# Kernel tuning notes

Hardware: AMD Instinct MI355X
Metric: run time of the kernel (lower is better)

## Reference

```python
import jax, jax.numpy as jnp
import numpy as np

D = 192          # embed_dim
DI = 2 * D       # d_inner (Mamba expand=2)
R = 12           # dt_rank = ceil(D / d_state)
N = 16           # d_state
DEPTH = 24
P = 16           # patch size
B = 4
SS, TS = 256, 128
PT = (TS // P) ** 2   # 64 template patches
PS = (SS // P) ** 2   # 256 search patches
L = PT + PS + 1       # 321 tokens (middle cls)


def setup_inputs() -> dict:
    key = jax.random.key(0)
    ks = jax.random.split(key, 24)
    f = lambda k, shp, s=0.02: (jax.random.normal(k, shp) * s).astype(jnp.float32)
    Alog = jnp.log(jnp.arange(1, N + 1, dtype=jnp.float32))  # S4D-real init
    Alog = jnp.tile(Alog, (DEPTH, DI, 1))
    return {
        "x_search": f(ks[0], (B, 3, SS, SS), 1.0),
        "x_template": f(ks[1], (B, 3, TS, TS), 1.0),
        "patch_w": f(ks[2], (D, 3, P, P)),
        "patch_b": jnp.zeros((D,), jnp.float32),
        "cls_token": f(ks[3], (1, 1, D)),
        "pos_embed": f(ks[4], (1, L, D)),
        "Win": f(ks[5], (DEPTH, 2 * DI, D)),
        "convw": f(ks[6], (DEPTH, DI, 4), 0.2),
        "convb": jnp.zeros((DEPTH, DI), jnp.float32),
        "Wx": f(ks[7], (DEPTH, R + 2 * N, DI)),
        "Wdt": f(ks[8], (DEPTH, DI, R), 0.1),
        "bdt": f(ks[9], (DEPTH, DI), 0.1),
        "Alog": Alog,
        "Dp": jnp.ones((DEPTH, DI), jnp.float32),
        "convw_b": f(ks[10], (DEPTH, DI, 4), 0.2),
        "convb_b": jnp.zeros((DEPTH, DI), jnp.float32),
        "Wx_b": f(ks[11], (DEPTH, R + 2 * N, DI)),
        "Wdt_b": f(ks[12], (DEPTH, DI, R), 0.1),
        "bdt_b": f(ks[13], (DEPTH, DI), 0.1),
        "Alog_b": Alog,
        "Dp_b": jnp.ones((DEPTH, DI), jnp.float32),
        "Wout": f(ks[14], (DEPTH, D, DI)),
        "normw": jnp.ones((DEPTH, D), jnp.float32),
        "normw_f": jnp.ones((D,), jnp.float32),
    }


def silu(x):
    return x * jax.nn.sigmoid(x)


def rmsnorm(x, w, eps=1e-5):
    return x * jax.lax.rsqrt(jnp.mean(x * x, -1, keepdims=True) + eps) * w


def patch_embed(x, w, b):
    # non-overlapping patch conv == blocked reshape + einsum
    Bn, C, H, W = x.shape
    xp = x.reshape(Bn, C, H // P, P, W // P, P)
    t = jnp.einsum('bcipjq,dcpq->bijd', xp, w)
    return t.reshape(Bn, (H // P) * (W // P), -1) + b


def causal_conv(u, w, b):
    # depthwise causal conv, kernel 4: u [B,DI,L], w [DI,4]
    Lx = u.shape[-1]
    up = jnp.pad(u, ((0, 0), (0, 0), (3, 0)))
    y = sum(w[:, k][None, :, None] * up[:, :, k:k + Lx] for k in range(4))
    return y + b[None, :, None]


def selective_scan(u, delta, A, Bm, Cm, Dp):
    # u, delta: [B,DI,L]; A: [DI,N]; Bm, Cm: [B,N,L]
    dA = jnp.exp(jnp.einsum('bdl,dn->lbdn', delta, A))
    dBu = jnp.einsum('bdl,bnl->lbdn', delta * u, Bm)

    def step(h, inp):
        dAt, dBut, ct = inp
        h = dAt * h + dBut
        return h, jnp.einsum('bdn,bn->bd', h, ct)

    h0 = jnp.zeros((u.shape[0], DI, N), u.dtype)
    _, ys = jax.lax.scan(step, h0, (dA, dBu, Cm.transpose(2, 0, 1)))
    y = ys.transpose(1, 2, 0)  # [B,DI,L]
    return y + Dp[None, :, None] * u


def _branch(x, z, convw, convb, Wx, Wdt, bdt, Alog, Dp):
    xc = silu(causal_conv(x, convw, convb))
    xdbl = jnp.einsum('bdl,ed->ble', xc, Wx)
    dt, Bm, Cm = xdbl[..., :R], xdbl[..., R:R + N], xdbl[..., R + N:]
    delta = jax.nn.softplus(jnp.einsum('blr,dr->bdl', dt, Wdt) + bdt[None, :, None])
    y = selective_scan(xc, delta, -jnp.exp(Alog), Bm.transpose(0, 2, 1),
                       Cm.transpose(0, 2, 1), Dp)
    return y * silu(z)


def _mixer(h, p):
    xz = jnp.einsum('bld,ed->ble', h, p['Win'])
    x = xz[..., :DI].transpose(0, 2, 1)   # [B,DI,L]
    z = xz[..., DI:].transpose(0, 2, 1)
    y = _branch(x, z, p['convw'], p['convb'], p['Wx'], p['Wdt'], p['bdt'],
                p['Alog'], p['Dp'])
    yb = _branch(x[..., ::-1], z[..., ::-1], p['convw_b'], p['convb_b'], p['Wx_b'],
                 p['Wdt_b'], p['bdt_b'], p['Alog_b'], p['Dp_b'])
    out = (y + yb[..., ::-1]) * 0.5  # bimamba v2 with if_divide_out
    return jnp.einsum('bdl,od->blo', out, p['Wout'])


def reference(x_search, x_template, patch_w, patch_b, cls_token, pos_embed,
              Win, convw, convb, Wx, Wdt, bdt, Alog, Dp,
              convw_b, convb_b, Wx_b, Wdt_b, bdt_b, Alog_b, Dp_b,
              Wout, normw, normw_f):
    ts = patch_embed(x_template, patch_w, patch_b)   # [B,64,D]
    ss = patch_embed(x_search, patch_w, patch_b)     # [B,256,D]
    tok = jnp.concatenate([ts, ss], 1)               # [B,320,D]
    mid = tok.shape[1] // 2
    cls = jnp.broadcast_to(cls_token, (tok.shape[0], 1, D))
    tok = jnp.concatenate([tok[:, :mid], cls, tok[:, mid:]], 1) + pos_embed

    lp = {'Win': Win, 'convw': convw, 'convb': convb, 'Wx': Wx, 'Wdt': Wdt,
          'bdt': bdt, 'Alog': Alog, 'Dp': Dp, 'convw_b': convw_b,
          'convb_b': convb_b, 'Wx_b': Wx_b, 'Wdt_b': Wdt_b, 'bdt_b': bdt_b,
          'Alog_b': Alog_b, 'Dp_b': Dp_b, 'Wout': Wout, 'normw': normw}

    def layer_step(carry, p):
        hidden, residual = carry
        residual = hidden + residual           # add
        hn = rmsnorm(residual, p['normw'])     # norm (fused_add_norm semantics)
        hidden = _mixer(hn, p)                 # mamba mixer
        return (hidden, residual), None

    (hidden, residual), _ = jax.lax.scan(layer_step, (tok, jnp.zeros_like(tok)), lp)
    return rmsnorm(hidden + residual, normw_f)   # final add + norm, [B,321,D]
```

## Files before the change

kernel.cpp:

```cpp
#include <hip/hip_runtime.h>
#include <math.h>

#define B_ 4
#define L_ 321
#define D_ 192
#define DI_ 384
#define E_ 768
#define R_ 12
#define N_ 16
#define DEPTH_ 24
#define XD 44

#define NC_ 21
#define LC_ 16

typedef __attribute__((ext_vector_type(8))) short bf16x8;
typedef __attribute__((ext_vector_type(4))) float f32x4;
typedef unsigned short ushort_t;

__device__ __forceinline__ float silu_f(float x) { return x / (1.f + __expf(-x)); }

__device__ __forceinline__ ushort_t f2bf(float x) {
    union { float f; unsigned u; } v; v.f = x;
    return (ushort_t)((v.u + 0x7fffu + ((v.u >> 16) & 1u)) >> 16);
}
__device__ __forceinline__ float bf2f(ushort_t h) {
    union { unsigned u; float f; } v; v.u = ((unsigned)h) << 16; return v.f;
}

__global__ void cvt_bf16(const float* __restrict__ src, ushort_t* __restrict__ dst, int n) {
    for (int i = blockIdx.x * blockDim.x + threadIdx.x; i < n; i += gridDim.x * blockDim.x)
        dst[i] = f2bf(src[i]);
}

__global__ void im2col_kernel(const float* __restrict__ xs, const float* __restrict__ xt,
                              ushort_t* __restrict__ pm) {
    int p_all = blockIdx.x % 320;
    int b = blockIdx.x / 320;
    const float* src; int i, j, W;
    if (p_all < 64) { int p = p_all; i = p >> 3; j = p & 7; W = 128; src = xt + (size_t)b*3*128*128; }
    else            { int p = p_all - 64; i = p >> 4; j = p & 15; W = 256; src = xs + (size_t)b*3*256*256; }
    ushort_t* dst = pm + (size_t)blockIdx.x * 768;
    for (int m = threadIdx.x; m < 768; m += blockDim.x) {
        int c = m >> 8, rem = m & 255, pp = rem >> 4, qq = rem & 15;
        dst[m] = f2bf(src[(size_t)(c*W + i*16 + pp)*W + j*16 + qq]);
    }
}

__global__ void tok_scatter(const float* __restrict__ tokmat, const float* __restrict__ pb,
                            const float* __restrict__ cls, const float* __restrict__ pos,
                            float* __restrict__ residual) {
    int blk = blockIdx.x;
    int b = blk / L_, t = blk % L_;
    int d = threadIdx.x;
    float v;
    if (t == 160) v = cls[d];
    else {
        int p = (t < 160) ? t : t - 1;
        v = tokmat[(size_t)(b*320 + p)*D_ + d] + pb[d];
    }
    residual[(size_t)(b*L_ + t)*D_ + d] = v + pos[t*D_ + d];
}

__global__ void rms0_kernel(const float* __restrict__ residual, const float* __restrict__ normw,
                            ushort_t* __restrict__ hn) {
    int row = blockIdx.x;
    int tid = threadIdx.x;
    __shared__ float red[256];
    float v = (tid < D_) ? residual[(size_t)row*D_ + tid] : 0.f;
    red[tid] = v * v;
    __syncthreads();
    for (int s = 128; s > 0; s >>= 1) { if (tid < s) red[tid] += red[tid + s]; __syncthreads(); }
    float scale = rsqrtf(red[0] / (float)D_ + 1e-5f);
    if (tid < D_) hn[(size_t)row*D_ + tid] = f2bf(v * scale * normw[tid]);
}

template<int WM, int WN, int MFR, int NFR, int CMODE>
__global__ __launch_bounds__(WM*WN*64) void mfma_gemm(const ushort_t* __restrict__ A,
                          const ushort_t* __restrict__ Bw,
                          float* __restrict__ Cf, ushort_t* __restrict__ Ch,
                          int M, int N, int K) {
    constexpr int BM = WM * MFR * 16;
    constexpr int BN = WN * NFR * 16;
    int bx = blockIdx.x, by = blockIdx.y;
    int wave = threadIdx.x >> 6, lane = threadIdx.x & 63;
    int wr = wave / WN, wc = wave % WN;
    int m0 = by * BM + wr * MFR * 16;
    int n0 = bx * BN + wc * NFR * 16;
    int lrow = lane & 15;
    int lk   = (lane >> 4) * 8;

    f32x4 acc[MFR][NFR];
#pragma unroll
    for (int i = 0; i < MFR; ++i)
#pragma unroll
        for (int j = 0; j < NFR; ++j) acc[i][j] = (f32x4){0.f, 0.f, 0.f, 0.f};

    for (int k0 = 0; k0 < K; k0 += 32) {
        bf16x8 a[MFR], b[NFR];
#pragma unroll
        for (int i = 0; i < MFR; ++i) {
            int r = m0 + i*16 + lrow; r = min(r, M - 1);
            a[i] = *(const bf16x8*)(A + (size_t)r*K + k0 + lk);
        }
#pragma unroll
        for (int jn = 0; jn < NFR; ++jn) {
            int c = n0 + jn*16 + lrow; c = min(c, N - 1);
            b[jn] = *(const bf16x8*)(Bw + (size_t)c*K + k0 + lk);
        }
#pragma unroll
        for (int i = 0; i < MFR; ++i)
#pragma unroll
            for (int jn = 0; jn < NFR; ++jn)
                acc[i][jn] = __builtin_amdgcn_mfma_f32_16x16x32_bf16(a[i], b[jn], acc[i][jn], 0, 0, 0);
    }

    int crow = (lane >> 4) * 4;
    int ccol = lane & 15;
#pragma unroll
    for (int i = 0; i < MFR; ++i)
#pragma unroll
        for (int jn = 0; jn < NFR; ++jn) {
            int c = n0 + jn*16 + ccol;
            if (c >= N) continue;
#pragma unroll
            for (int j = 0; j < 4; ++j) {
                int r = m0 + i*16 + crow + j;
                if (r < M) {
                    if (CMODE == 0) Cf[(size_t)r*N + c] = acc[i][jn][j];
                    else            Ch[(size_t)r*N + c] = f2bf(acc[i][jn][j]);
                }
            }
        }
}

__global__ void conv_kernel(const ushort_t* __restrict__ xz,
                            const float* __restrict__ cw, const float* __restrict__ cb,
                            const float* __restrict__ cwb, const float* __restrict__ cbb,
                            ushort_t* __restrict__ xc_f, ushort_t* __restrict__ xc_b) {
    int blk = blockIdx.x;
    int b = blk / L_, l = blk % L_;
    int d = threadIdx.x;
    const ushort_t* xbase = xz + (size_t)b*L_*E_ + d;
    float acc = cb[d];
#pragma unroll
    for (int k = 0; k < 4; ++k) {
        int t = l - 3 + k;
        if (t >= 0) acc = fmaf(cw[d*4 + k], bf2f(xbase[(size_t)t*E_]), acc);
    }
    xc_f[(size_t)(b*L_ + l)*DI_ + d] = f2bf(silu_f(acc));
    float accb = cbb[d];
#pragma unroll
    for (int k = 0; k < 4; ++k) {
        int t = l - 3 + k;
        if (t >= 0) accb = fmaf(cwb[d*4 + k], bf2f(xbase[(size_t)(L_ - 1 - t)*E_]), accb);
    }
    xc_b[(size_t)(b*L_ + l)*DI_ + d] = f2bf(silu_f(accb));
}

__global__ __launch_bounds__(384) void scan1_xdbl(
    const ushort_t* __restrict__ xc_f, const ushort_t* __restrict__ xc_b,
    const ushort_t* __restrict__ Wxf, const ushort_t* __restrict__ Wxbw,
    const float* __restrict__ Wdt, const float* __restrict__ bdt,
    const float* __restrict__ Wdtb, const float* __restrict__ bdtb,
    const float* __restrict__ Alog, const float* __restrict__ Alogb,
    float* __restrict__ xdbl_f, float* __restrict__ xdbl_b,
    float* __restrict__ hloc, float* __restrict__ aprod) {
    int c = blockIdx.x, b = blockIdx.y, br = blockIdx.z;
    int tid = threadIdx.x, wave = tid >> 6, lane = tid & 63;
    const ushort_t* xc = br ? xc_b : xc_f;
    const ushort_t* Wx = br ? Wxbw : Wxf;
    const float* Wd = br ? Wdtb : Wdt;
    const float* bd = br ? bdtb : bdt;
    const float* Al = br ? Alogb : Alog;
    float* xdout = br ? xdbl_b : xdbl_f;

    __shared__ float sxd[LC_][48];
    int lbeg = c * LC_;
    int len = min(lbeg + LC_, L_) - lbeg;

    if (wave < 3) {
        int lrow = lane & 15, lk = (lane >> 4) * 8;
        int arow = b * L_ + min(lbeg + lrow, L_ - 1);
        int bcol = min(wave * 16 + lrow, XD - 1);
        f32x4 acc = (f32x4){0.f, 0.f, 0.f, 0.f};
        for (int k0 = 0; k0 < DI_; k0 += 32) {
            bf16x8 a  = *(const bf16x8*)(xc + (size_t)arow * DI_ + k0 + lk);
            bf16x8 bw = *(const bf16x8*)(Wx + (size_t)bcol * DI_ + k0 + lk);
            acc = __builtin_amdgcn_mfma_f32_16x16x32_bf16(a, bw, acc, 0, 0, 0);
        }
        int crow = (lane >> 4) * 4, ccol = lane & 15;
#pragma unroll
        for (int j = 0; j < 4; ++j) sxd[crow + j][wave * 16 + ccol] = acc[j];
    }

    int d = tid;
    float u[LC_];
    if (len == LC_) {
#pragma unroll
        for (int l2 = 0; l2 < LC_; ++l2)
            u[l2] = bf2f(xc[((size_t)b*L_ + lbeg + l2)*DI_ + d]);
    }
    __syncthreads();

    for (int idx = tid; idx < len * XD; idx += 384) {
        int l2 = idx / XD, col = idx % XD;
        xdout[((size_t)b*L_ + lbeg + l2)*XD + col] = sxd[l2][col];
    }

    float wreg[R_];
#pragma unroll
    for (int r = 0; r < R_; ++r) wreg[r] = Wd[d*R_ + r];
    float bdv = bd[d];
    float a[N_];
#pragma unroll
    for (int n = 0; n < N_; ++n) a[n] = -__expf(Al[d*N_ + n]);
    float h[N_], ap[N_];
#pragma unroll
    for (int n = 0; n < N_; ++n) { h[n] = 0.f; ap[n] = 1.f; }

    auto step = [&](int l2, float uv) {
        float dacc = bdv;
#pragma unroll
        for (int r = 0; r < R_; ++r) dacc = fmaf(wreg[r], sxd[l2][r], dacc);
        float dv = fmaxf(dacc, 0.f) + log1pf(__expf(-fabsf(dacc)));
        float du = dv * uv;
#pragma unroll
        for (int n = 0; n < N_; ++n) {
            float e = __expf(dv * a[n]);
            h[n] = fmaf(e, h[n], du * sxd[l2][R_ + n]);
            ap[n] *= e;
        }
    };
    if (len == LC_) {
#pragma unroll 4
        for (int l2 = 0; l2 < LC_; ++l2) step(l2, u[l2]);
    } else {
        for (int l2 = 0; l2 < len; ++l2)
            step(l2, bf2f(xc[((size_t)b*L_ + lbeg + l2)*DI_ + d]));
    }
    size_t base = (((size_t)(b*2 + br)*NC_ + c)*N_)*DI_ + d;
#pragma unroll
    for (int n = 0; n < N_; ++n) {
        hloc[base + (size_t)n*DI_]  = h[n];
        aprod[base + (size_t)n*DI_] = ap[n];
    }
}

__global__ void scan_combine(const float* __restrict__ hloc, const float* __restrict__ aprod,
                             float* __restrict__ hin) {
    int g = blockIdx.x * blockDim.x + threadIdx.x;
    int bb = g / (N_ * DI_);
    int rem = g % (N_ * DI_);
    float hrun = 0.f;
    for (int c = 0; c < NC_; ++c) {
        size_t idx = ((size_t)bb*NC_ + c)*N_*DI_ + rem;
        hin[idx] = hrun;
        hrun = fmaf(aprod[idx], hrun, hloc[idx]);
    }
}

__global__ __launch_bounds__(192) void scan_part3(
                           const ushort_t* __restrict__ xc_f, const ushort_t* __restrict__ xc_b,
                           const float* __restrict__ xdbl_f, const float* __restrict__ xdbl_b,
                           const float* __restrict__ Wdt, const float* __restrict__ bdt,
                           const float* __restrict__ Wdtb, const float* __restrict__ bdtb,
                           const ushort_t* __restrict__ xz,
                           const float* __restrict__ Alog, const float* __restrict__ Alogb,
                           const float* __restrict__ Dpf, const float* __restrict__ Dpb,
                           const float* __restrict__ hin,
                           float* __restrict__ y_f, float* __restrict__ y_b) {
    int c = blockIdx.x, b = blockIdx.y >> 1, half = blockIdx.y & 1, br = blockIdx.z;
    int tid = threadIdx.x;
    int d = half * 192 + tid;
    const ushort_t* xc = br ? xc_b : xc_f;
    const float* xd = br ? xdbl_b : xdbl_f;
    const float* Wd = br ? Wdtb : Wdt;
    const float* bd = br ? bdtb : bdt;
    const float* Al = br ? Alogb : Alog;
    const float* Dpp = br ? Dpb : Dpf;
    float* y = br ? y_b : y_f;
    __shared__ float sdt[LC_][R_];
    __shared__ float sB[LC_][N_];
    __shared__ float sC[LC_][N_];
    int lbeg = c * LC_;
    int len = min(lbeg + LC_, L_) - lbeg;
    for (int idx = tid; idx < len*N_; idx += 192) {
        int l2 = idx >> 4, n = idx & 15;
        size_t row = (size_t)b*L_ + lbeg + l2;
        sB[l2][n] = xd[row*XD + R_ + n];
        sC[l2][n] = xd[row*XD + R_ + N_ + n];
    }
    for (int idx = tid; idx < len*R_; idx += 192) {
        int l2 = idx / R_, r = idx % R_;
        sdt[l2][r] = xd[((size_t)b*L_ + lbeg + l2)*XD + r];
    }
    __syncthreads();
    float wreg[R_];
#pragma unroll
    for (int r = 0; r < R_; ++r) wreg[r] = Wd[d*R_ + r];
    float bdv = bd[d];
    float a[N_];
#pragma unroll
    for (int n = 0; n < N_; ++n) a[n] = -__expf(Al[d*N_ + n]);
    float h[N_];
    size_t hbase = (((size_t)(b*2 + br)*NC_ + c)*N_)*DI_ + d;
#pragma unroll
    for (int n = 0; n < N_; ++n) h[n] = hin[hbase + (size_t)n*DI_];
    float dpv = Dpp[d];

    auto step = [&](int l2, float uv) {
        float dacc = bdv;
#pragma unroll
        for (int r = 0; r < R_; ++r) dacc = fmaf(wreg[r], sdt[l2][r], dacc);
        float dv = fmaxf(dacc, 0.f) + log1pf(__expf(-fabsf(dacc)));
        float du = dv * uv;
        float yv = 0.f;
#pragma unroll
        for (int n = 0; n < N_; ++n) {
            float e = __expf(dv * a[n]);
            h[n] = fmaf(e, h[n], du * sB[l2][n]);
            yv = fmaf(h[n], sC[l2][n], yv);
        }
        yv = fmaf(dpv, uv, yv);
        int lo = br ? (L_ - 1 - (lbeg + l2)) : (lbeg + l2);
        float zv = bf2f(xz[((size_t)b*L_ + lo)*E_ + DI_ + d]);
        y[((size_t)b*L_ + lo)*DI_ + d] = yv * silu_f(zv);
    };
    if (len == LC_) {
        float u[LC_];
#pragma unroll
        for (int l2 = 0; l2 < LC_; ++l2)
            u[l2] = bf2f(xc[((size_t)b*L_ + lbeg + l2)*DI_ + d]);
#pragma unroll 4
        for (int l2 = 0; l2 < LC_; ++l2) step(l2, u[l2]);
    } else {
        for (int l2 = 0; l2 < len; ++l2)
            step(l2, bf2f(xc[((size_t)b*L_ + lbeg + l2)*DI_ + d]));
    }
}

template<bool LAST>
__global__ __launch_bounds__(256) void outproj_fused(
    const float* __restrict__ yf, const float* __restrict__ yb,
    const ushort_t* __restrict__ Ww,
    float* __restrict__ residual, const float* __restrict__ nw,
    ushort_t* __restrict__ hn, float* __restrict__ outp) {
    const int M = B_*L_, Nn = D_, K = DI_;
    int wave = threadIdx.x >> 6, lane = threadIdx.x & 63;
    int m0 = blockIdx.x * 16;
    int n0 = wave * 48;
    int lrow = lane & 15, lk = (lane >> 4) * 8;

    f32x4 acc[3];
#pragma unroll
    for (int jn = 0; jn < 3; ++jn) acc[jn] = (f32x4){0.f, 0.f, 0.f, 0.f};

    for (int k0 = 0; k0 < K; k0 += 32) {
        int r = min(m0 + lrow, M - 1);
        const float* p0 = yf + (size_t)r*K + k0 + lk;
        const float* p1 = yb + (size_t)r*K + k0 + lk;
        bf16x8 a;
#pragma unroll
        for (int j = 0; j < 8; ++j) a[j] = (short)f2bf(0.5f*(p0[j] + p1[j]));
        bf16x8 b[3];
#pragma unroll
        for (int jn = 0; jn < 3; ++jn) {
            int c = n0 + jn*16 + lrow;
            b[jn] = *(const bf16x8*)(Ww + (size_t)c*K + k0 + lk);
        }
#pragma unroll
        for (int jn = 0; jn < 3; ++jn)
            acc[jn] = __builtin_amdgcn_mfma_f32_16x16x32_bf16(a, b[jn], acc[jn], 0, 0, 0);
    }

    int crow = (lane >> 4) * 4, ccol = lane & 15;
    float resv[4][3];
    float sq[4] = {0.f, 0.f, 0.f, 0.f};
#pragma unroll
    for (int j = 0; j < 4; ++j) {
        int r = m0 + crow + j;
        bool ok = r < M;
#pragma unroll
        for (int jn = 0; jn < 3; ++jn) {
            int c = n0 + jn*16 + ccol;
            float v = ok ? (residual[(size_t)r*Nn + c] + acc[jn][j]) : 0.f;
            resv[j][jn] = v;
            sq[j] = fmaf(v, v, sq[j]);
        }
    }
#pragma unroll
    for (int m = 1; m < 16; m <<= 1)
#pragma unroll
        for (int j = 0; j < 4; ++j) sq[j] += __shfl_xor(sq[j], m, 64);

    __shared__ float part[16][4];
    if (ccol == 0) {
#pragma unroll
        for (int j = 0; j < 4; ++j) part[crow + j][wave] = sq[j];
    }
    __syncthreads();
#pragma unroll
    for (int j = 0; j < 4; ++j) {
        int r = m0 + crow + j;
        if (r >= M) continue;
        int rt = crow + j;
        float tot = part[rt][0] + part[rt][1] + part[rt][2] + part[rt][3];
        float scale = rsqrtf(tot / (float)Nn + 1e-5f);
#pragma unroll
        for (int jn = 0; jn < 3; ++jn) {
            int c = n0 + jn*16 + ccol;
            float v = resv[j][jn];
            if (LAST) {
                outp[(size_t)r*Nn + c] = v * scale * nw[c];
            } else {
                residual[(size_t)r*Nn + c] = v;
                hn[(size_t)r*Nn + c] = f2bf(v * scale * nw[c]);
            }
        }
    }
}

extern "C" void kernel_launch(void* const* d_in, const int* in_sizes, int n_in,
                              void* d_out, int out_size, void* d_ws, size_t ws_size,
                              hipStream_t stream) {
    const float* xs     = (const float*)d_in[0];
    const float* xt     = (const float*)d_in[1];
    const float* pw     = (const float*)d_in[2];
    const float* pb     = (const float*)d_in[3];
    const float* cls    = (const float*)d_in[4];
    const float* pos    = (const float*)d_in[5];
    const float* Win    = (const float*)d_in[6];
    const float* convw  = (const float*)d_in[7];
    const float* convb  = (const float*)d_in[8];
    const float* Wx     = (const float*)d_in[9];
    const float* Wdt    = (const float*)d_in[10];
    const float* bdt    = (const float*)d_in[11];
    const float* Alog   = (const float*)d_in[12];
    const float* Dp     = (const float*)d_in[13];
    const float* convwb = (const float*)d_in[14];
    const float* convbb = (const float*)d_in[15];
    const float* Wxb    = (const float*)d_in[16];
    const float* Wdtb   = (const float*)d_in[17];
    const float* bdtb   = (const float*)d_in[18];
    const float* Alogb  = (const float*)d_in[19];
    const float* Dpb    = (const float*)d_in[20];
    const float* Wout   = (const float*)d_in[21];
    const float* normw  = (const float*)d_in[22];
    const float* normwf = (const float*)d_in[23];
    float* out = (float*)d_out;

    float* ws = (float*)d_ws;
    size_t off = 0;
    auto alloc = [&](size_t nfloats) { float* p = ws + off; off += nfloats; return p; };
    const size_t BL = (size_t)B_ * L_;
    const size_t CHNK = (size_t)B_ * 2 * NC_ * N_ * DI_;

    float*    residual = alloc(BL * D_);
    ushort_t* hn_bf    = (ushort_t*)alloc(BL * D_ / 2);
    ushort_t* xzb_bf   = (ushort_t*)alloc(BL * E_ / 2);
    ushort_t* xcf_bf   = (ushort_t*)alloc(BL * DI_ / 2);
    ushort_t* xcb_bf   = (ushort_t*)alloc(BL * DI_ / 2);
    float*    xdbl_f   = alloc(BL * XD);
    float*    xdbl_b   = alloc(BL * XD);
    float*    y_f      = alloc(BL * DI_);
    float*    y_b      = alloc(BL * DI_);
    float*    hloc     = alloc(CHNK);
    float*    aprod    = alloc(CHNK);
    float*    hin      = alloc(CHNK);
    ushort_t* pw_bf    = (ushort_t*)alloc((size_t)D_ * 768 / 2);
    ushort_t* Win_bf   = (ushort_t*)alloc((size_t)DEPTH_ * E_ * D_ / 2);
    ushort_t* Wx_bf    = (ushort_t*)alloc((size_t)DEPTH_ * XD * DI_ / 2);
    ushort_t* Wxb_bf   = (ushort_t*)alloc((size_t)DEPTH_ * XD * DI_ / 2);
    ushort_t* Wout_bf  = (ushort_t*)alloc((size_t)DEPTH_ * D_ * DI_ / 2);
    (void)ws_size; (void)in_sizes; (void)n_in; (void)out_size;

    cvt_bf16<<<dim3(64),   dim3(256), 0, stream>>>(pw,   pw_bf,   D_ * 768);
    cvt_bf16<<<dim3(2048), dim3(256), 0, stream>>>(Win,  Win_bf,  DEPTH_ * E_ * D_);
    cvt_bf16<<<dim3(512),  dim3(256), 0, stream>>>(Wx,   Wx_bf,   DEPTH_ * XD * DI_);
    cvt_bf16<<<dim3(512),  dim3(256), 0, stream>>>(Wxb,  Wxb_bf,  DEPTH_ * XD * DI_);
    cvt_bf16<<<dim3(1024), dim3(256), 0, stream>>>(Wout, Wout_bf, DEPTH_ * D_ * DI_);

    ushort_t* pmat   = (ushort_t*)y_f;
    float*    tokmat = y_b;
    im2col_kernel<<<dim3(B_ * 320), dim3(256), 0, stream>>>(xs, xt, pmat);
    mfma_gemm<2, 2, 2, 2, 0><<<dim3(3, 20), dim3(256), 0, stream>>>(
        pmat, pw_bf, tokmat, nullptr, B_ * 320, D_, 768);
    tok_scatter<<<dim3(B_ * L_), dim3(192), 0, stream>>>(tokmat, pb, cls, pos, residual);
    rms0_kernel<<<dim3((int)BL), dim3(256), 0, stream>>>(residual, normw, hn_bf);

    for (int layer = 0; layer < DEPTH_; ++layer) {
        const ushort_t* Win_l  = Win_bf  + (size_t)layer * E_ * D_;
        const ushort_t* Wx_l   = Wx_bf   + (size_t)layer * XD * DI_;
        const ushort_t* Wxb_l  = Wxb_bf  + (size_t)layer * XD * DI_;
        const ushort_t* Wout_l = Wout_bf + (size_t)layer * D_ * DI_;
        const float* cw_l    = convw  + (size_t)layer * DI_ * 4;
        const float* cb_l    = convb  + (size_t)layer * DI_;
        const float* cwb_l   = convwb + (size_t)layer * DI_ * 4;
        const float* cbb_l   = convbb + (size_t)layer * DI_;
        const float* Wdt_l   = Wdt    + (size_t)layer * DI_ * R_;
        const float* Wdtb_l  = Wdtb   + (size_t)layer * DI_ * R_;
        const float* bdt_l   = bdt    + (size_t)layer * DI_;
        const float* bdtb_l  = bdtb   + (size_t)layer * DI_;
        const float* Alog_l  = Alog   + (size_t)layer * DI_ * N_;
        const float* Alogb_l = Alogb  + (size_t)layer * DI_ * N_;
        const float* Dp_l    = Dp     + (size_t)layer * DI_;
        const float* Dpb_l   = Dpb    + (size_t)layer * DI_;

        mfma_gemm<2, 2, 2, 2, 1><<<dim3(12, 21), dim3(256), 0, stream>>>(
            hn_bf, Win_l, nullptr, xzb_bf, (int)BL, E_, D_);
        conv_kernel<<<dim3((int)BL), dim3(DI_), 0, stream>>>(
            xzb_bf, cw_l, cb_l, cwb_l, cbb_l, xcf_bf, xcb_bf);
        scan1_xdbl<<<dim3(NC_, B_, 2), dim3(384), 0, stream>>>(
            xcf_bf, xcb_bf, Wx_l, Wxb_l, Wdt_l, bdt_l, Wdtb_l, bdtb_l,
            Alog_l, Alogb_l, xdbl_f, xdbl_b, hloc, aprod);
        scan_combine<<<dim3((B_*2*N_*DI_)/256), dim3(256), 0, stream>>>(hloc, aprod, hin);
        scan_part3<<<dim3(NC_, B_ * 2, 2), dim3(192), 0, stream>>>(
            xcf_bf, xcb_bf, xdbl_f, xdbl_b, Wdt_l, bdt_l, Wdtb_l, bdtb_l, xzb_bf,
            Alog_l, Alogb_l, Dp_l, Dpb_l, hin, y_f, y_b);
        if (layer < DEPTH_ - 1) {
            outproj_fused<false><<<dim3(81), dim3(256), 0, stream>>>(
                y_f, y_b, Wout_l, residual, normw + (size_t)(layer + 1) * D_, hn_bf, nullptr);
        } else {
            outproj_fused<true><<<dim3(81), dim3(256), 0, stream>>>(
                y_f, y_b, Wout_l, residual, normwf, nullptr, out);
        }
    }
}
```

Before: 1.831 ms.

## Fuse scan combine into chunk-scan via last-block atomic, store y in bf16

```diff
diff --git a/kernel.cpp b/kernel.cpp
--- a/kernel.cpp
+++ b/kernel.cpp
@@ -28,9 +28,33 @@
     union { unsigned u; float f; } v; v.u = ((unsigned)h) << 16; return v.f;
 }
 
-__global__ void cvt_bf16(const float* __restrict__ src, ushort_t* __restrict__ dst, int n) {
-    for (int i = blockIdx.x * blockDim.x + threadIdx.x; i < n; i += gridDim.x * blockDim.x)
-        dst[i] = f2bf(src[i]);
+__global__ void cvt_bf16_multi(const float* __restrict__ s0, ushort_t* __restrict__ d0, int n0,
+                               const float* __restrict__ s1, ushort_t* __restrict__ d1, int n1,
+                               const float* __restrict__ s2, ushort_t* __restrict__ d2, int n2,
+                               const float* __restrict__ s3, ushort_t* __restrict__ d3, int n3,
+                               const float* __restrict__ s4, ushort_t* __restrict__ d4, int n4) {
+    int total = n0 + n1 + n2 + n3 + n4;
+    for (int i = blockIdx.x * blockDim.x + threadIdx.x; i < total; i += gridDim.x * blockDim.x) {
+        int j = i;
+        const float* s; ushort_t* d;
+        if (j < n0) { s = s0; d = d0; }
+        else { j -= n0;
+            if (j < n1) { s = s1; d = d1; }
+            else { j -= n1;
+                if (j < n2) { s = s2; d = d2; }
+                else { j -= n2;
+                    if (j < n3) { s = s3; d = d3; }
+                    else { j -= n3; s = s4; d = d4; }
+                }
+            }
+        }
+        d[j] = f2bf(s[j]);
+    }
+}
+
+__global__ void zero_cnt(int* __restrict__ c, int n) {
+    int i = blockIdx.x * blockDim.x + threadIdx.x;
+    if (i < n) c[i] = 0;
 }
 
 __global__ void im2col_kernel(const float* __restrict__ xs, const float* __restrict__ xt,
@@ -47,9 +71,10 @@
     }
 }
 
-__global__ void tok_scatter(const float* __restrict__ tokmat, const float* __restrict__ pb,
-                            const float* __restrict__ cls, const float* __restrict__ pos,
-                            float* __restrict__ residual) {
+__global__ void tok_rms(const float* __restrict__ tokmat, const float* __restrict__ pb,
+                        const float* __restrict__ cls, const float* __restrict__ pos,
+                        const float* __restrict__ normw,
+                        float* __restrict__ residual, ushort_t* __restrict__ hn) {
     int blk = blockIdx.x;
     int b = blk / L_, t = blk % L_;
     int d = threadIdx.x;
@@ -59,20 +84,18 @@
         int p = (t < 160) ? t : t - 1;
         v = tokmat[(size_t)(b*320 + p)*D_ + d] + pb[d];
     }
-    residual[(size_t)(b*L_ + t)*D_ + d] = v + pos[t*D_ + d];
-}
-
-__global__ void rms0_kernel(const float* __restrict__ residual, const float* __restrict__ normw,
-                            ushort_t* __restrict__ hn) {
-    int row = blockIdx.x;
-    int tid = threadIdx.x;
-    __shared__ float red[256];
-    float v = (tid < D_) ? residual[(size_t)row*D_ + tid] : 0.f;
-    red[tid] = v * v;
+    v += pos[t*D_ + d];
+    residual[(size_t)blk*D_ + d] = v;
+    float sq = v * v;
+#pragma unroll
+    for (int m = 1; m < 64; m <<= 1) sq += __shfl_xor(sq, m, 64);
+    __shared__ float part[3];
+    int wave = d >> 6, lane = d & 63;
+    if (lane == 0) part[wave] = sq;
     __syncthreads();
-    for (int s = 128; s > 0; s >>= 1) { if (tid < s) red[tid] += red[tid + s]; __syncthreads(); }
-    float scale = rsqrtf(red[0] / (float)D_ + 1e-5f);
-    if (tid < D_) hn[(size_t)row*D_ + tid] = f2bf(v * scale * normw[tid]);
+    float tot = part[0] + part[1] + part[2];
+    float scale = rsqrtf(tot / (float)D_ + 1e-5f);
+    hn[(size_t)blk*D_ + d] = f2bf(v * scale * normw[d]);
 }
 
 template<int WM, int WN, int MFR, int NFR, int CMODE>
@@ -165,7 +188,8 @@
     const float* __restrict__ Wdtb, const float* __restrict__ bdtb,
     const float* __restrict__ Alog, const float* __restrict__ Alogb,
     float* __restrict__ xdbl_f, float* __restrict__ xdbl_b,
-    float* __restrict__ hloc, float* __restrict__ aprod) {
+    float* __restrict__ hloc, float* __restrict__ aprod,
+    float* __restrict__ hin, int* __restrict__ cnt) {
     int c = blockIdx.x, b = blockIdx.y, br = blockIdx.z;
     int tid = threadIdx.x, wave = tid >> 6, lane = tid & 63;
     const ushort_t* xc = br ? xc_b : xc_f;
@@ -176,6 +200,7 @@
     float* xdout = br ? xdbl_b : xdbl_f;
 
     __shared__ float sxd[LC_][48];
+    __shared__ int sLast;
     int lbeg = c * LC_;
     int len = min(lbeg + LC_, L_) - lbeg;
 
@@ -245,18 +270,25 @@
         hloc[base + (size_t)n*DI_]  = h[n];
         aprod[base + (size_t)n*DI_] = ap[n];
     }
-}
-
-__global__ void scan_combine(const float* __restrict__ hloc, const float* __restrict__ aprod,
-                             float* __restrict__ hin) {
-    int g = blockIdx.x * blockDim.x + threadIdx.x;
-    int bb = g / (N_ * DI_);
-    int rem = g % (N_ * DI_);
-    float hrun = 0.f;
-    for (int c = 0; c < NC_; ++c) {
-        size_t idx = ((size_t)bb*NC_ + c)*N_*DI_ + rem;
-        hin[idx] = hrun;
-        hrun = fmaf(aprod[idx], hrun, hloc[idx]);
+
+    __threadfence();
+    if (tid == 0) sLast = (atomicAdd(&cnt[b*2 + br], 1) == NC_ - 1);
+    __syncthreads();
+    if (sLast) {
+        __threadfence();
+        float hr[N_];
+#pragma unroll
+        for (int n = 0; n < N_; ++n) hr[n] = 0.f;
+        size_t bb = ((size_t)(b*2 + br)*NC_)*N_*DI_ + d;
+        for (int cc = 0; cc < NC_; ++cc) {
+            size_t cb2 = bb + (size_t)cc*N_*DI_;
+#pragma unroll
+            for (int n = 0; n < N_; ++n) {
+                size_t ix = cb2 + (size_t)n*DI_;
+                hin[ix] = hr[n];
+                hr[n] = fmaf(aprod[ix], hr[n], hloc[ix]);
+            }
+        }
     }
 }
 
@@ -269,7 +301,7 @@
                            const float* __restrict__ Alog, const float* __restrict__ Alogb,
                            const float* __restrict__ Dpf, const float* __restrict__ Dpb,
                            const float* __restrict__ hin,
-                           float* __restrict__ y_f, float* __restrict__ y_b) {
+                           ushort_t* __restrict__ y_f, ushort_t* __restrict__ y_b) {
     int c = blockIdx.x, b = blockIdx.y >> 1, half = blockIdx.y & 1, br = blockIdx.z;
     int tid = threadIdx.x;
     int d = half * 192 + tid;
@@ -279,7 +311,7 @@
     const float* bd = br ? bdtb : bdt;
     const float* Al = br ? Alogb : Alog;
     const float* Dpp = br ? Dpb : Dpf;
-    float* y = br ? y_b : y_f;
+    ushort_t* y = br ? y_b : y_f;
     __shared__ float sdt[LC_][R_];
     __shared__ float sB[LC_][N_];
     __shared__ float sC[LC_][N_];
@@ -325,7 +357,7 @@
         yv = fmaf(dpv, uv, yv);
         int lo = br ? (L_ - 1 - (lbeg + l2)) : (lbeg + l2);
         float zv = bf2f(xz[((size_t)b*L_ + lo)*E_ + DI_ + d]);
-        y[((size_t)b*L_ + lo)*DI_ + d] = yv * silu_f(zv);
+        y[((size_t)b*L_ + lo)*DI_ + d] = f2bf(yv * silu_f(zv));
     };
     if (len == LC_) {
         float u[LC_];
@@ -342,7 +374,7 @@
 
 template<bool LAST>
 __global__ __launch_bounds__(256) void outproj_fused(
-    const float* __restrict__ yf, const float* __restrict__ yb,
+    const ushort_t* __restrict__ yf, const ushort_t* __restrict__ yb,
     const ushort_t* __restrict__ Ww,
     float* __restrict__ residual, const float* __restrict__ nw,
     ushort_t* __restrict__ hn, float* __restrict__ outp) {
@@ -358,11 +390,12 @@
 
     for (int k0 = 0; k0 < K; k0 += 32) {
         int r = min(m0 + lrow, M - 1);
-        const float* p0 = yf + (size_t)r*K + k0 + lk;
-        const float* p1 = yb + (size_t)r*K + k0 + lk;
+        bf16x8 vf = *(const bf16x8*)(yf + (size_t)r*K + k0 + lk);
+        bf16x8 vb = *(const bf16x8*)(yb + (size_t)r*K + k0 + lk);
         bf16x8 a;
 #pragma unroll
-        for (int j = 0; j < 8; ++j) a[j] = (short)f2bf(0.5f*(p0[j] + p1[j]));
+        for (int j = 0; j < 8; ++j)
+            a[j] = (short)f2bf(0.5f*(bf2f((ushort_t)vf[j]) + bf2f((ushort_t)vb[j])));
         bf16x8 b[3];
 #pragma unroll
         for (int jn = 0; jn < 3; ++jn) {
@@ -463,11 +496,12 @@
     ushort_t* xcb_bf   = (ushort_t*)alloc(BL * DI_ / 2);
     float*    xdbl_f   = alloc(BL * XD);
     float*    xdbl_b   = alloc(BL * XD);
-    float*    y_f      = alloc(BL * DI_);
-    float*    y_b      = alloc(BL * DI_);
+    ushort_t* y_f      = (ushort_t*)alloc(BL * DI_ / 2);
+    ushort_t* y_b      = (ushort_t*)alloc(BL * DI_ / 2);
     float*    hloc     = alloc(CHNK);
     float*    aprod    = alloc(CHNK);
     float*    hin      = alloc(CHNK);
+    int*      cnt      = (int*)alloc(DEPTH_ * 8);
     ushort_t* pw_bf    = (ushort_t*)alloc((size_t)D_ * 768 / 2);
     ushort_t* Win_bf   = (ushort_t*)alloc((size_t)DEPTH_ * E_ * D_ / 2);
     ushort_t* Wx_bf    = (ushort_t*)alloc((size_t)DEPTH_ * XD * DI_ / 2);
@@ -475,19 +509,21 @@
     ushort_t* Wout_bf  = (ushort_t*)alloc((size_t)DEPTH_ * D_ * DI_ / 2);
     (void)ws_size; (void)in_sizes; (void)n_in; (void)out_size;
 
-    cvt_bf16<<<dim3(64),   dim3(256), 0, stream>>>(pw,   pw_bf,   D_ * 768);
-    cvt_bf16<<<dim3(2048), dim3(256), 0, stream>>>(Win,  Win_bf,  DEPTH_ * E_ * D_);
-    cvt_bf16<<<dim3(512),  dim3(256), 0, stream>>>(Wx,   Wx_bf,   DEPTH_ * XD * DI_);
-    cvt_bf16<<<dim3(512),  dim3(256), 0, stream>>>(Wxb,  Wxb_bf,  DEPTH_ * XD * DI_);
-    cvt_bf16<<<dim3(1024), dim3(256), 0, stream>>>(Wout, Wout_bf, DEPTH_ * D_ * DI_);
-
-    ushort_t* pmat   = (ushort_t*)y_f;
-    float*    tokmat = y_b;
+    zero_cnt<<<dim3(1), dim3(256), 0, stream>>>(cnt, DEPTH_ * 8);
+
+    cvt_bf16_multi<<<dim3(2048), dim3(256), 0, stream>>>(
+        pw,   pw_bf,   D_ * 768,
+        Win,  Win_bf,  DEPTH_ * E_ * D_,
+        Wx,   Wx_bf,   DEPTH_ * XD * DI_,
+        Wxb,  Wxb_bf,  DEPTH_ * XD * DI_,
+        Wout, Wout_bf, DEPTH_ * D_ * DI_);
+
+    ushort_t* pmat   = (ushort_t*)hloc;
+    float*    tokmat = aprod;
     im2col_kernel<<<dim3(B_ * 320), dim3(256), 0, stream>>>(xs, xt, pmat);
     mfma_gemm<2, 2, 2, 2, 0><<<dim3(3, 20), dim3(256), 0, stream>>>(
         pmat, pw_bf, tokmat, nullptr, B_ * 320, D_, 768);
-    tok_scatter<<<dim3(B_ * L_), dim3(192), 0, stream>>>(tokmat, pb, cls, pos, residual);
-    rms0_kernel<<<dim3((int)BL), dim3(256), 0, stream>>>(residual, normw, hn_bf);
+    tok_rms<<<dim3(B_ * L_), dim3(192), 0, stream>>>(tokmat, pb, cls, pos, normw, residual, hn_bf);
 
     for (int layer = 0; layer < DEPTH_; ++layer) {
         const ushort_t* Win_l  = Win_bf  + (size_t)layer * E_ * D_;
@@ -513,8 +549,7 @@
             xzb_bf, cw_l, cb_l, cwb_l, cbb_l, xcf_bf, xcb_bf);
         scan1_xdbl<<<dim3(NC_, B_, 2), dim3(384), 0, stream>>>(
             xcf_bf, xcb_bf, Wx_l, Wxb_l, Wdt_l, bdt_l, Wdtb_l, bdtb_l,
-            Alog_l, Alogb_l, xdbl_f, xdbl_b, hloc, aprod);
-        scan_combine<<<dim3((B_*2*N_*DI_)/256), dim3(256), 0, stream>>>(hloc, aprod, hin);
+            Alog_l, Alogb_l, xdbl_f, xdbl_b, hloc, aprod, hin, cnt + layer * 8);
         scan_part3<<<dim3(NC_, B_ * 2, 2), dim3(192), 0, stream>>>(
             xcf_bf, xcb_bf, xdbl_f, xdbl_b, Wdt_l, bdt_l, Wdtb_l, bdtb_l, xzb_bf,
             Alog_l, Alogb_l, Dp_l, Dpb_l, hin, y_f, y_b);
```

Measured after the change: 2.744 ms. 49.9% more time.
